# Performance work log

Measured on AMD Instinct MI355X. Metric: run time of the kernel, lower is better.

The kernel has to match this reference:

```python
import jax, jax.numpy as jnp
import numpy as np

B, S, D = 2, 1024, 2048
H, KV, HD = 16, 4, 128
GROUPS = H // KV
THETA = 10000.0


def act_quant(xr, xi):
    # per-token 8-bit absmax quantization over last dim, joint scale for re/im, STE
    amax = jnp.maximum(jnp.max(jnp.abs(xr), -1, keepdims=True),
                       jnp.max(jnp.abs(xi), -1, keepdims=True))
    s = 127.0 / jnp.maximum(amax, 1e-5)
    qr = jnp.clip(jnp.round(xr * s), -128, 127) / s
    qi = jnp.clip(jnp.round(xi * s), -128, 127) / s
    return xr + jax.lax.stop_gradient(qr - xr), xi + jax.lax.stop_gradient(qi - xi)


def weight_quant(wr, wi):
    # Fairy+-i direction quantization: each weight -> scale * d, d in {+1,-1,+i,-i}; STE
    mag = jnp.mean(jnp.sqrt(wr * wr + wi * wi))
    use_re = jnp.abs(wr) >= jnp.abs(wi)
    qr = jnp.where(use_re, jnp.sign(wr) * mag, 0.0)
    qi = jnp.where(use_re, 0.0, jnp.sign(wi) * mag)
    return wr + jax.lax.stop_gradient(qr - wr), wi + jax.lax.stop_gradient(qi - wi)


def complex_linear(xr, xi, wr, wi):
    xr, xi = act_quant(xr, xi)
    wr, wi = weight_quant(wr, wi)
    o_re = xr @ wr - xi @ wi
    o_im = xr @ wi + xi @ wr
    return o_re, o_im


def rotate_half(x):
    h = x.shape[-1] // 2
    return jnp.concatenate([-x[..., h:], x[..., :h]], axis=-1)


def rope_tables():
    inv_freq = 1.0 / (THETA ** (jnp.arange(0, HD, 2, dtype=jnp.float32) / HD))
    pos = jnp.arange(S, dtype=jnp.float32)
    freqs = pos[:, None] * inv_freq[None, :]          # [S, HD/2]
    emb = jnp.concatenate([freqs, freqs], axis=-1)    # [S, HD]
    return jnp.cos(emb)[None, None], jnp.sin(emb)[None, None]  # [1,1,S,HD]


def _heads(x, n):
    # [B,S,n*HD] -> [B,n,S,HD]
    return x.reshape(B, S, n, HD).transpose(0, 2, 1, 3)


def _attn(hidden_real, hidden_imag, wq_re, wq_im, wk_re, wk_im,
          wv_re, wv_im, wo_re, wo_im):
    q_re, q_im = complex_linear(hidden_real, hidden_imag, wq_re, wq_im)
    k_re, k_im = complex_linear(hidden_real, hidden_imag, wk_re, wk_im)
    v_re, v_im = complex_linear(hidden_real, hidden_imag, wv_re, wv_im)

    q_re, q_im = _heads(q_re, H), _heads(q_im, H)      # [B,H,S,HD]
    k_re, k_im = _heads(k_re, KV), _heads(k_im, KV)    # [B,KV,S,HD]
    v_re, v_im = _heads(v_re, KV), _heads(v_im, KV)

    cos, sin = rope_tables()
    # RoPE applied only to real components of q and k
    q_re = q_re * cos + rotate_half(q_re) * sin
    k_re = k_re * cos + rotate_half(k_re) * sin

    # GQA repeat
    k_re = jnp.repeat(k_re, GROUPS, axis=1)
    k_im = jnp.repeat(k_im, GROUPS, axis=1)
    v_re = jnp.repeat(v_re, GROUPS, axis=1)
    v_im = jnp.repeat(v_im, GROUPS, axis=1)

    # real scores = Re(q . conj(k)) = q_re.k_re + q_im.k_im
    scores = (jnp.einsum('bhqd,bhkd->bhqk', q_re, k_re) +
              jnp.einsum('bhqd,bhkd->bhqk', q_im, k_im)) / jnp.sqrt(jnp.float32(HD))
    causal = jnp.tril(jnp.ones((S, S), dtype=bool))
    scores = jnp.where(causal[None, None], scores, jnp.finfo(scores.dtype).min)
    attn = jax.nn.softmax(scores, axis=-1)

    o_re = jnp.einsum('bhqk,bhkd->bhqd', attn, v_re)
    o_im = jnp.einsum('bhqk,bhkd->bhqd', attn, v_im)
    o_re = o_re.transpose(0, 2, 1, 3).reshape(B, S, H * HD)
    o_im = o_im.transpose(0, 2, 1, 3).reshape(B, S, H * HD)

    out_re, out_im = complex_linear(o_re, o_im, wo_re, wo_im)
    return jnp.stack([out_re, out_im])  # [2,B,S,D]


def setup_inputs() -> dict:
    key = jax.random.key(0)
    ks = jax.random.split(key, 12)
    w = lambda k, shp: jax.random.normal(k, shp, dtype=jnp.float32) * 0.02
    return {
        'hidden_real': jax.random.normal(ks[0], (B, S, D), dtype=jnp.float32),
        'hidden_imag': jax.random.normal(ks[1], (B, S, D), dtype=jnp.float32),
        'wq_re': w(ks[2], (D, H * HD)), 'wq_im': w(ks[3], (D, H * HD)),
        'wk_re': w(ks[4], (D, KV * HD)), 'wk_im': w(ks[5], (D, KV * HD)),
        'wv_re': w(ks[6], (D, KV * HD)), 'wv_im': w(ks[7], (D, KV * HD)),
        'wo_re': w(ks[8], (H * HD, D)), 'wo_im': w(ks[9], (H * HD, D)),
    }


def reference(hidden_real, hidden_imag, wq_re, wq_im, wk_re, wk_im,
              wv_re, wv_im, wo_re, wo_im):
    return _attn(hidden_real, hidden_imag, wq_re, wq_im, wk_re, wk_im,
                 wv_re, wv_im, wo_re, wo_im)
```

## Files before the change

### kernel.cpp

```cpp
#include <hip/hip_runtime.h>
#include <stdint.h>

#define B_   2
#define S_   1024
#define D_   2048
#define H_   16
#define KV_  4
#define HD_  128
#define NTOK (B_ * S_)
#define QD   (H_ * HD_)
#define KD   (KV_ * HD_)

using i32x4  = __attribute__((ext_vector_type(4)))  int;
using i32x16 = __attribute__((ext_vector_type(16))) int;
using f32x4  = __attribute__((ext_vector_type(4)))  float;
using bf16x8 = __attribute__((ext_vector_type(8)))  short;

#define LN1E4_OVER_64 0.14391156831212725f

__device__ __forceinline__ float bf2f(uint16_t u) { return __uint_as_float((uint32_t)u << 16); }
__device__ __forceinline__ uint16_t f2bf(float f) {
    uint32_t u = __float_as_uint(f);
    return (uint16_t)((u + 0x7FFFu + ((u >> 16) & 1u)) >> 16);
}

__global__ __launch_bounds__(256)
void act_quant_i8_kernel(const float* __restrict__ xr, const float* __restrict__ xi,
                         int8_t* __restrict__ qr, int8_t* __restrict__ qi,
                         float* __restrict__ invs)
{
    const int tok = blockIdx.x, t = threadIdx.x;
    const float* pr = xr + (size_t)tok * 2048 + t * 8;
    const float* pi = xi + (size_t)tok * 2048 + t * 8;
    float4 r0 = *(const float4*)pr, r1 = *(const float4*)(pr + 4);
    float4 i0 = *(const float4*)pi, i1 = *(const float4*)(pi + 4);
    float am = fmaxf(fmaxf(fmaxf(fabsf(r0.x), fabsf(r0.y)), fmaxf(fabsf(r0.z), fabsf(r0.w))),
                     fmaxf(fmaxf(fabsf(r1.x), fabsf(r1.y)), fmaxf(fabsf(r1.z), fabsf(r1.w))));
    am = fmaxf(am, fmaxf(fmaxf(fmaxf(fabsf(i0.x), fabsf(i0.y)), fmaxf(fabsf(i0.z), fabsf(i0.w))),
                         fmaxf(fmaxf(fabsf(i1.x), fabsf(i1.y)), fmaxf(fabsf(i1.z), fabsf(i1.w)))));
    __shared__ float red[256];
    red[t] = am;
    __syncthreads();
    for (int st = 128; st > 0; st >>= 1) {
        if (t < st) red[t] = fmaxf(red[t], red[t + st]);
        __syncthreads();
    }
    const float s = 127.0f / fmaxf(red[0], 1e-5f);
    if (t == 0) invs[tok] = 1.0f / s;
#define Q8(x) ((uint32_t)(uint8_t)(int8_t)(int)fminf(fmaxf(rintf((x) * s), -128.f), 127.f))
    uint32_t a0 = Q8(r0.x) | (Q8(r0.y) << 8) | (Q8(r0.z) << 16) | (Q8(r0.w) << 24);
    uint32_t a1 = Q8(r1.x) | (Q8(r1.y) << 8) | (Q8(r1.z) << 16) | (Q8(r1.w) << 24);
    uint32_t b0 = Q8(i0.x) | (Q8(i0.y) << 8) | (Q8(i0.z) << 16) | (Q8(i0.w) << 24);
    uint32_t b1 = Q8(i1.x) | (Q8(i1.y) << 8) | (Q8(i1.z) << 16) | (Q8(i1.w) << 24);
#undef Q8
    *(uint32_t*)(qr + (size_t)tok * 2048 + t * 8)     = a0;
    *(uint32_t*)(qr + (size_t)tok * 2048 + t * 8 + 4) = a1;
    *(uint32_t*)(qi + (size_t)tok * 2048 + t * 8)     = b0;
    *(uint32_t*)(qi + (size_t)tok * 2048 + t * 8 + 4) = b1;
}

__global__ __launch_bounds__(256)
void decode_kernel(const float* __restrict__ wr, const float* __restrict__ wi,
                   int N, int8_t* __restrict__ psr, int8_t* __restrict__ psi,
                   int8_t* __restrict__ pnsi, int n_off, float* __restrict__ mag_out)
{
    __shared__ alignas(16) int8_t tr[3][64][80];
    __shared__ float red[256];
    const int n0 = blockIdx.x * 64, k0 = blockIdx.y * 64;
    float msum = 0.f;
    for (int idx = threadIdx.x; idx < 4096; idx += 256) {
        int j = idx & 63, i = idx >> 6;
        size_t g = (size_t)(k0 + i) * N + n0 + j;
        float a = wr[g], b = wi[g];
        msum += sqrtf(a * a + b * b);
        int8_t sr, si;
        if (fabsf(a) >= fabsf(b)) {
            sr = (a > 0.f) ? 1 : ((a < 0.f) ? -1 : 0);
            si = 0;
        } else {
            sr = 0;
            si = (b > 0.f) ? 1 : ((b < 0.f) ? -1 : 0);
        }
        tr[0][j][i] = sr;
        tr[1][j][i] = si;
        tr[2][j][i] = (int8_t)(-si);
    }
    red[threadIdx.x] = msum;
    __syncthreads();
    for (int st = 128; st > 0; st >>= 1) {
        if (threadIdx.x < st) red[threadIdx.x] += red[threadIdx.x + st];
        __syncthreads();
    }
    if (threadIdx.x == 0) atomicAdd(mag_out, red[0]);
    int8_t* planes[3] = { psr, psi, pnsi };
    for (int idx = threadIdx.x; idx < 768; idx += 256) {
        int p = idx >> 8, rem = idx & 255, n = rem >> 2, c = rem & 3;
        int4 v = *(const int4*)&tr[p][n][c * 16];
        *(int4*)(planes[p] + (size_t)(n_off + n0 + n) * 2048 + k0 + c * 16) = v;
    }
}

__device__ __forceinline__ void async_copy16(const void* g, void* l) {
    __builtin_amdgcn_global_load_lds((const __attribute__((address_space(1))) void*)g,
                                     (__attribute__((address_space(3))) void*)l, 16, 0, 0);
}

template <int MODE>
__global__ __launch_bounds__(512, 4)
void gemm_i8_kernel(const int8_t* __restrict__ axr, const int8_t* __restrict__ axi,
                    const int8_t* __restrict__ bsr, const int8_t* __restrict__ bsi,
                    const int8_t* __restrict__ bnsi,
                    int Nout, const float* __restrict__ invs,
                    const float* __restrict__ mag_sums,
                    float magc0, float magc1, float magc2,
                    float* o_re, float* o_im,
                    uint16_t* kbr, uint16_t* kbi, uint16_t* vbr, uint16_t* vbi)
{
    __shared__ alignas(16) int8_t smem[2][5 * 8192];
    const int tid = threadIdx.x;
    const int wav = tid >> 6, lane = tid & 63;
    const int tileM = blockIdx.y * 128, tileN = blockIdx.x * 128;
    const int wm = wav & 1, wn = wav >> 1;
    const int K = 2048;

    const int8_t* gplane[5] = { axr, axi, bsr, bsi, bnsi };
    const int     rbase[5]  = { tileM, tileM, tileN, tileN, tileN };

    i32x16 acc_re[2] = {};
    i32x16 acc_im[2] = {};

    auto issue_tile = [&](int k0, int buf) {
#pragma unroll
        for (int i = 0; i < 5; ++i) {
            int q = wav + 8 * i;
            int pl = q >> 3, seg = q & 7;
            int c = seg >> 1, m0 = (seg & 1) << 6;
            const int8_t* g = gplane[pl] + (size_t)(rbase[pl] + m0 + lane) * K + k0 + c * 16;
            int8_t* l = &smem[buf][pl * 8192 + (c * 128 + m0) * 16];
            async_copy16(g, l);
        }
    };

    issue_tile(0, 0);
    issue_tile(64, 1);

    for (int k = 0; k < 32; ++k) {
        if (k == 31) { asm volatile("s_waitcnt vmcnt(0)" ::: "memory"); }
        else         { asm volatile("s_waitcnt vmcnt(5)" ::: "memory"); }
        asm volatile("s_barrier" ::: "memory");
        const int8_t* sb = smem[k & 1];
#pragma unroll
        for (int s = 0; s < 2; ++s) {
            const int cc = 2 * s + (lane >> 5);
            const int rA = wm * 64 + (lane & 31);
            const int rB = wn * 32 + (lane & 31);
            i32x4 fxr[2], fxi[2], fsr, fsi, fns;
#pragma unroll
            for (int mb = 0; mb < 2; ++mb) {
                int off = (cc * 128 + rA + mb * 32) * 16;
                fxr[mb] = *(const i32x4*)&sb[0 * 8192 + off];
                fxi[mb] = *(const i32x4*)&sb[1 * 8192 + off];
            }
            {
                int off = (cc * 128 + rB) * 16;
                fsr = *(const i32x4*)&sb[2 * 8192 + off];
                fsi = *(const i32x4*)&sb[3 * 8192 + off];
                fns = *(const i32x4*)&sb[4 * 8192 + off];
            }
#pragma unroll
            for (int mb = 0; mb < 2; ++mb) {
                acc_re[mb] = __builtin_amdgcn_mfma_i32_32x32x32_i8(fxr[mb], fsr, acc_re[mb], 0, 0, 0);
                acc_re[mb] = __builtin_amdgcn_mfma_i32_32x32x32_i8(fxi[mb], fns, acc_re[mb], 0, 0, 0);
                acc_im[mb] = __builtin_amdgcn_mfma_i32_32x32x32_i8(fxr[mb], fsi, acc_im[mb], 0, 0, 0);
                acc_im[mb] = __builtin_amdgcn_mfma_i32_32x32x32_i8(fxi[mb], fsr, acc_im[mb], 0, 0, 0);
            }
        }
        asm volatile("s_barrier" ::: "memory");
        if (k + 2 < 32) issue_tile((k + 2) * 64, k & 1);
    }

    const int ln31 = lane & 31, lq = lane >> 5;
    const int gn = tileN + wn * 32 + ln31;
    float mag;
    if (MODE == 0)
        mag = (gn < 2048) ? mag_sums[0] * magc0
            : (gn < 2560) ? mag_sums[1] * magc1
                          : mag_sums[2] * magc2;
    else
        mag = mag_sums[0] * magc0;
#pragma unroll
    for (int mb = 0; mb < 2; ++mb) {
#pragma unroll
        for (int r = 0; r < 16; ++r) {
            const int row = (r & 3) + 8 * (r >> 2) + 4 * lq;
            const int gm = tileM + wm * 64 + mb * 32 + row;
            const float sc = mag * invs[gm];
            const float re = (float)acc_re[mb][r] * sc;
            const float im = (float)acc_im[mb][r] * sc;
            if (MODE == 1) {
                o_re[(size_t)gm * Nout + gn] = re;
                o_im[(size_t)gm * Nout + gn] = im;
            } else {
                const int s = gm & (S_ - 1), bb = gm >> 10;
                if (gn < 2048) {
                    o_re[(size_t)gm * 2048 + gn] = re;
                    o_im[(size_t)gm * 2048 + gn] = im;
                } else if (gn < 2560) {
                    int c = gn - 2048, kvh = c >> 7, d = c & 127;
                    size_t off = ((size_t)(bb * KV_ + kvh) * S_ + s) * 128 + d;
                    kbr[off] = f2bf(re);
                    kbi[off] = f2bf(im);
                } else {
                    int c = gn - 2560, kvh = c >> 7, d = c & 127;
                    size_t off = ((size_t)(bb * KV_ + kvh) * S_ + s) * 128 + d;
                    vbr[off] = f2bf(re);
                    vbi[off] = f2bf(im);
                }
            }
        }
    }
}

__global__ __launch_bounds__(256)
void rope_q_kernel(const float* __restrict__ q_re, const float* __restrict__ q_im,
                   uint16_t* __restrict__ qb_re, uint16_t* __restrict__ qb_im)
{
    int gidx = blockIdx.x * 256 + threadIdx.x;
    int j = gidx & 15, h = (gidx >> 4) & 15, tok = gidx >> 8;
    int s = tok & (S_ - 1), b = tok >> 10;
    int d0 = j * 4;
    size_t ib = (size_t)tok * 2048 + h * 128;
    float4 r0 = *(const float4*)&q_re[ib + d0];
    float4 r1 = *(const float4*)&q_re[ib + d0 + 64];
    float4 i0 = *(const float4*)&q_im[ib + d0];
    float4 i1 = *(const float4*)&q_im[ib + d0 + 64];
    float ro0[4], ro1[4];
    float rv0[4] = { r0.x, r0.y, r0.z, r0.w };
    float rv1[4] = { r1.x, r1.y, r1.z, r1.w };
#pragma unroll
    for (int t = 0; t < 4; ++t) {
        float f = __expf(-(float)(d0 + t) * LN1E4_OVER_64);
        float sn, c;
        __sincosf((float)s * f, &sn, &c);
        ro0[t] = rv0[t] * c - rv1[t] * sn;
        ro1[t] = rv1[t] * c + rv0[t] * sn;
    }
    size_t ob = ((size_t)(b * H_ + h) * S_ + s) * 128;
    ushort4 w;
    w = (ushort4){ f2bf(ro0[0]), f2bf(ro0[1]), f2bf(ro0[2]), f2bf(ro0[3]) };
    *(ushort4*)&qb_re[ob + d0] = w;
    w = (ushort4){ f2bf(ro1[0]), f2bf(ro1[1]), f2bf(ro1[2]), f2bf(ro1[3]) };
    *(ushort4*)&qb_re[ob + d0 + 64] = w;
    w = (ushort4){ f2bf(i0.x), f2bf(i0.y), f2bf(i0.z), f2bf(i0.w) };
    *(ushort4*)&qb_im[ob + d0] = w;
    w = (ushort4){ f2bf(i1.x), f2bf(i1.y), f2bf(i1.z), f2bf(i1.w) };
    *(ushort4*)&qb_im[ob + d0 + 64] = w;
}

__global__ __launch_bounds__(256)
void rope_k_kernel(uint16_t* __restrict__ kb_re)
{
    int gidx = blockIdx.x * 256 + threadIdx.x;
    int j = gidx & 15, kvh = (gidx >> 4) & 3;
    int rest = gidx >> 6;
    int s = rest & (S_ - 1), b = rest >> 10;
    int d0 = j * 4;
    size_t base = ((size_t)(b * KV_ + kvh) * S_ + s) * 128;
    ushort4 u0 = *(const ushort4*)&kb_re[base + d0];
    ushort4 u1 = *(const ushort4*)&kb_re[base + d0 + 64];
    float rv0[4] = { bf2f(u0.x), bf2f(u0.y), bf2f(u0.z), bf2f(u0.w) };
    float rv1[4] = { bf2f(u1.x), bf2f(u1.y), bf2f(u1.z), bf2f(u1.w) };
    float ro0[4], ro1[4];
#pragma unroll
    for (int t = 0; t < 4; ++t) {
        float f = __expf(-(float)(d0 + t) * LN1E4_OVER_64);
        float sn, c;
        __sincosf((float)s * f, &sn, &c);
        ro0[t] = rv0[t] * c - rv1[t] * sn;
        ro1[t] = rv1[t] * c + rv0[t] * sn;
    }
    *(ushort4*)&kb_re[base + d0]      = (ushort4){ f2bf(ro0[0]), f2bf(ro0[1]), f2bf(ro0[2]), f2bf(ro0[3]) };
    *(ushort4*)&kb_re[base + d0 + 64] = (ushort4){ f2bf(ro1[0]), f2bf(ro1[1]), f2bf(ro1[2]), f2bf(ro1[3]) };
}

__global__ __launch_bounds__(256)
void vtrans_kernel(const uint16_t* __restrict__ vbr, const uint16_t* __restrict__ vbi,
                   uint16_t* __restrict__ vtr, uint16_t* __restrict__ vti)
{
    __shared__ uint16_t t[32][36];
    const int pl = blockIdx.z & 1, bk = blockIdx.z >> 1;
    const int s0 = blockIdx.x * 32, d0 = blockIdx.y * 32;
    const uint16_t* src = (pl ? vbi : vbr) + ((size_t)bk * S_) * 128;
    uint16_t*       dst = (pl ? vti : vtr) + ((size_t)bk * 128) * S_;
    const int r = threadIdx.x >> 3, c = (threadIdx.x & 7) * 4;
    *(ushort4*)&t[r][c] = *(const ushort4*)&src[(size_t)(s0 + r) * 128 + d0 + c];
    __syncthreads();
    ushort4 o = (ushort4){ t[c][r], t[c + 1][r], t[c + 2][r], t[c + 3][r] };
    *(ushort4*)&dst[(size_t)(d0 + r) * S_ + s0 + c] = o;
}

__global__ __launch_bounds__(256)
void attn_mfma_kernel(const uint16_t* __restrict__ qb_re, const uint16_t* __restrict__ qb_im,
                      const uint16_t* __restrict__ kb_re, const uint16_t* __restrict__ kb_im,
                      const uint16_t* __restrict__ vt_re, const uint16_t* __restrict__ vt_im,
                      float* __restrict__ o_re, float* __restrict__ o_im)
{
    __shared__ alignas(16) uint16_t sbuf[2][16384];
    __shared__ alignas(16) uint16_t sp[4][16][40];

    const int tid = threadIdx.x;
    const int w = tid >> 6, lane = tid & 63;
    const int r16 = lane & 15, q4 = lane >> 4;
    const int qt = gridDim.x - 1 - blockIdx.x;
    const int h = blockIdx.y, b = blockIdx.z;
    const int kvh = h >> 2;
    const int q0 = qt * 64, qw0 = q0 + w * 16;

    bf16x8 qfr[4], qfi[4];
    {
        const size_t qbase = ((size_t)(b * H_ + h) * S_ + qw0 + r16) * 128;
#pragma unroll
        for (int ks = 0; ks < 4; ++ks) {
            const int col = ks * 32 + q4 * 8;
            qfr[ks] = *(const bf16x8*)&qb_re[qbase + col];
            qfi[ks] = *(const bf16x8*)&qb_im[qbase + col];
        }
    }

    f32x4 oa[2][8] = {};
    float m_r[4] = { -3e38f, -3e38f, -3e38f, -3e38f };
    float l_r[4] = { 0.f, 0.f, 0.f, 0.f };

    const size_t kgbase0 = (size_t)(b * KV_ + kvh) * S_ * 128;
    const uint16_t* vre = vt_re + (size_t)(b * KV_ + kvh) * 128 * (size_t)S_;
    const uint16_t* vim = vt_im + (size_t)(b * KV_ + kvh) * 128 * (size_t)S_;

    const uint16_t* kp[4];
    const uint16_t* vp[4];
#pragma unroll
    for (int i = 0; i < 4; ++i) {
        const int kch = (i & 1) * 8 + w * 2 + (lane >> 5);
        kp[i] = ((i >> 1) ? kb_im : kb_re) + kgbase0 + (size_t)(lane & 31) * 128 + kch * 8;
        const int vch = (i & 1) * 2 + (w >> 1);
        const int vd  = ((w & 1) << 6) | lane;
        vp[i] = ((i >> 1) ? vim : vre) + (size_t)vd * S_ + vch * 8;
    }

    auto issue_tile = [&](int kt, int buf) {
#pragma unroll
        for (int i = 0; i < 4; ++i)
            async_copy16(kp[i] + (size_t)kt * 4096, &sbuf[buf][w * 512 + i * 2048]);
#pragma unroll
        for (int i = 0; i < 4; ++i)
            async_copy16(vp[i] + (size_t)kt * 32, &sbuf[buf][8192 + w * 512 + i * 2048]);
    };

    const int nk = (q0 + 64) >> 5;

    issue_tile(0, 0);
    issue_tile(1, 1);

    for (int k = 0; k < nk; ++k) {
        if (k == nk - 1) { asm volatile("s_waitcnt vmcnt(0)" ::: "memory"); }
        else             { asm volatile("s_waitcnt vmcnt(8)" ::: "memory"); }
        asm volatile("s_barrier" ::: "memory");
        const uint16_t* sb = sbuf[k & 1];
        const int c0 = k << 5;

        if (c0 <= qw0 + 15) {
            f32x4 sc[2] = {};
#pragma unroll
            for (int cblk = 0; cblk < 2; ++cblk) {
                const int krow = cblk * 16 + r16;
#pragma unroll
                for (int ks = 0; ks < 4; ++ks) {
                    const int koff = (ks * 4 + q4) * 256 + krow * 8;
                    bf16x8 kr = *(const bf16x8*)&sb[koff];
                    bf16x8 ki = *(const bf16x8*)&sb[4096 + koff];
                    sc[cblk] = __builtin_amdgcn_mfma_f32_16x16x32_bf16(qfr[ks], kr, sc[cblk], 0, 0, 0);
                    sc[cblk] = __builtin_amdgcn_mfma_f32_16x16x32_bf16(qfi[ks], ki, sc[cblk], 0, 0, 0);
                }
            }
#pragma unroll
            for (int cblk = 0; cblk < 2; ++cblk)
#pragma unroll
                for (int reg = 0; reg < 4; ++reg) {
                    float sval = sc[cblk][reg] * 0.08838834764831845f;
                    const int rowg = qw0 + q4 * 4 + reg;
                    const int colg = c0 + cblk * 16 + r16;
                    if (colg > rowg) sval = -3e38f;
                    sc[cblk][reg] = sval;
                }
            float al[4];
#pragma unroll
            for (int reg = 0; reg < 4; ++reg) {
                float mx = fmaxf(sc[0][reg], sc[1][reg]);
#pragma unroll
                for (int msk = 1; msk < 16; msk <<= 1) mx = fmaxf(mx, __shfl_xor(mx, msk));
                const float mn = fmaxf(m_r[reg], mx);
                al[reg] = __expf(m_r[reg] - mn);
                const float p0 = __expf(sc[0][reg] - mn);
                const float p1 = __expf(sc[1][reg] - mn);
                sc[0][reg] = p0; sc[1][reg] = p1;
                float rs = p0 + p1;
#pragma unroll
                for (int msk = 1; msk < 16; msk <<= 1) rs += __shfl_xor(rs, msk);
                l_r[reg] = l_r[reg] * al[reg] + rs;
                m_r[reg] = mn;
            }
#pragma unroll
            for (int cblk = 0; cblk < 2; ++cblk)
#pragma unroll
                for (int reg = 0; reg < 4; ++reg)
                    sp[w][q4 * 4 + reg][cblk * 16 + r16] = f2bf(sc[cblk][reg]);
#pragma unroll
            for (int dblk = 0; dblk < 8; ++dblk)
#pragma unroll
                for (int reg = 0; reg < 4; ++reg) {
                    oa[0][dblk][reg] *= al[reg];
                    oa[1][dblk][reg] *= al[reg];
                }
            bf16x8 pf = *(const bf16x8*)&sp[w][r16][q4 * 8];
#pragma unroll
            for (int dblk = 0; dblk < 8; ++dblk) {
                const int voff = 8192 + q4 * 1024 + (dblk * 16 + r16) * 8;
                bf16x8 vr = *(const bf16x8*)&sb[voff];
                bf16x8 vi = *(const bf16x8*)&sb[4096 + voff];
                oa[0][dblk] = __builtin_amdgcn_mfma_f32_16x16x32_bf16(pf, vr, oa[0][dblk], 0, 0, 0);
                oa[1][dblk] = __builtin_amdgcn_mfma_f32_16x16x32_bf16(pf, vi, oa[1][dblk], 0, 0, 0);
            }
        }

        asm volatile("s_barrier" ::: "memory");
        if (k + 2 < nk) issue_tile(k + 2, k & 1);
    }

    float inv[4];
#pragma unroll
    for (int reg = 0; reg < 4; ++reg) inv[reg] = 1.f / l_r[reg];
#pragma unroll
    for (int dblk = 0; dblk < 8; ++dblk) {
        const int col = h * 128 + dblk * 16 + r16;
#pragma unroll
        for (int reg = 0; reg < 4; ++reg) {
            const size_t tok = (size_t)b * S_ + qw0 + q4 * 4 + reg;
            o_re[tok * 2048 + col] = oa[0][dblk][reg] * inv[reg];
            o_im[tok * 2048 + col] = oa[1][dblk][reg] * inv[reg];
        }
    }
}

extern "C" void kernel_launch(void* const* d_in, const int* in_sizes, int n_in,
                              void* d_out, int out_size, void* d_ws, size_t ws_size,
                              hipStream_t stream)
{
    const float* hr    = (const float*)d_in[0];
    const float* hi    = (const float*)d_in[1];
    const float* wq_re = (const float*)d_in[2];
    const float* wq_im = (const float*)d_in[3];
    const float* wk_re = (const float*)d_in[4];
    const float* wk_im = (const float*)d_in[5];
    const float* wv_re = (const float*)d_in[6];
    const float* wv_im = (const float*)d_in[7];
    const float* wo_re = (const float*)d_in[8];
    const float* wo_im = (const float*)d_in[9];
    float* out = (float*)d_out;
    char*  base = (char*)d_ws;

    const size_t MB4  = (size_t)2048 * 2048;
    const size_t QKVP = (size_t)3072 * 2048;
    const size_t KVE  = (size_t)B_ * KV_ * S_ * 128;

    float*   mags   = (float*)(base);
    float*   invs1  = (float*)(base + 1024);
    float*   invs2  = (float*)(base + 9216);
    int8_t*  xr_q   = (int8_t*)(base + 32768);
    int8_t*  xi_q   = xr_q + MB4;
    int8_t*  qkv_sr = xi_q + MB4;
    int8_t*  qkv_si = qkv_sr + QKVP;
    int8_t*  qkv_ns = qkv_si + QKVP;
    int8_t*  wo_sr  = qkv_ns + QKVP;
    int8_t*  wo_si  = wo_sr + MB4;
    int8_t*  wo_ns  = wo_si + MB4;
    float*   q_re   = (float*)(wo_ns + MB4);
    float*   q_im   = q_re + MB4;
    uint16_t* kb_re = (uint16_t*)(q_im + MB4);
    uint16_t* kb_im = kb_re + KVE;
    uint16_t* vb_re = kb_im + KVE;
    uint16_t* vb_im = vb_re + KVE;
    uint16_t* vt_re = (uint16_t*)xr_q;
    uint16_t* vt_im = (uint16_t*)xi_q;
    uint16_t* qb_re = (uint16_t*)qkv_sr;
    uint16_t* qb_im = (uint16_t*)(qkv_sr + 8388608);

    hipMemsetAsync(mags, 0, 16, stream);

    decode_kernel<<<dim3(32, 32), 256, 0, stream>>>(wq_re, wq_im, 2048, qkv_sr, qkv_si, qkv_ns, 0,    mags + 0);
    decode_kernel<<<dim3(8, 32),  256, 0, stream>>>(wk_re, wk_im, 512,  qkv_sr, qkv_si, qkv_ns, 2048, mags + 1);
    decode_kernel<<<dim3(8, 32),  256, 0, stream>>>(wv_re, wv_im, 512,  qkv_sr, qkv_si, qkv_ns, 2560, mags + 2);
    decode_kernel<<<dim3(32, 32), 256, 0, stream>>>(wo_re, wo_im, 2048, wo_sr, wo_si, wo_ns, 0,       mags + 3);

    act_quant_i8_kernel<<<NTOK, 256, 0, stream>>>(hr, hi, xr_q, xi_q, invs1);

    gemm_i8_kernel<0><<<dim3(24, 16), 512, 0, stream>>>(
        xr_q, xi_q, qkv_sr, qkv_si, qkv_ns, 0, invs1, mags,
        1.0f / (float)((size_t)D_ * QD), 1.0f / (float)((size_t)D_ * KD), 1.0f / (float)((size_t)D_ * KD),
        q_re, q_im, kb_re, kb_im, vb_re, vb_im);

    rope_q_kernel<<<NTOK * H_ * 16 / 256, 256, 0, stream>>>(q_re, q_im, qb_re, qb_im);
    rope_k_kernel<<<NTOK * KV_ * 16 / 256, 256, 0, stream>>>(kb_re);
    vtrans_kernel<<<dim3(S_ / 32, 128 / 32, B_ * KV_ * 2), 256, 0, stream>>>(vb_re, vb_im, vt_re, vt_im);

    attn_mfma_kernel<<<dim3(S_ / 64, H_, B_), 256, 0, stream>>>(
        qb_re, qb_im, kb_re, kb_im, vt_re, vt_im, q_re, q_im);

    act_quant_i8_kernel<<<NTOK, 256, 0, stream>>>(q_re, q_im, xr_q, xi_q, invs2);

    gemm_i8_kernel<1><<<dim3(16, 16), 512, 0, stream>>>(
        xr_q, xi_q, wo_sr, wo_si, wo_ns, 2048, invs2, mags + 3,
        1.0f / (float)((size_t)QD * D_), 0.f, 0.f,
        out, out + MB4, nullptr, nullptr, nullptr, nullptr);
}
```

Baseline: 486.5 us.

## Drop negated weight plane and retile int8 complex GEMM to 64x128

The decode kernel no longer writes a third negated-imaginary weight plane. The GEMM instead keeps separate accumulators for xr·wr and xi·wi and subtracts them in the epilogue, which cuts weight-plane traffic and LDS footprint per tile. The GEMM tile also shrinks from 128x128 with 512 threads to 64x128 with 256 threads, doubling the grid in M and changing the occupancy hint. The cost is one extra accumulator set per wave, which raises register pressure, and less A/B reuse per block.

```diff
diff --git a/kernel.cpp b/kernel.cpp
--- a/kernel.cpp
+++ b/kernel.cpp
@@ -62,9 +62,9 @@
 __global__ __launch_bounds__(256)
 void decode_kernel(const float* __restrict__ wr, const float* __restrict__ wi,
                    int N, int8_t* __restrict__ psr, int8_t* __restrict__ psi,
-                   int8_t* __restrict__ pnsi, int n_off, float* __restrict__ mag_out)
-{
-    __shared__ alignas(16) int8_t tr[3][64][80];
+                   int n_off, float* __restrict__ mag_out)
+{
+    __shared__ alignas(16) int8_t tr[2][64][80];
     __shared__ float red[256];
     const int n0 = blockIdx.x * 64, k0 = blockIdx.y * 64;
     float msum = 0.f;
@@ -83,7 +83,6 @@
         }
         tr[0][j][i] = sr;
         tr[1][j][i] = si;
-        tr[2][j][i] = (int8_t)(-si);
     }
     red[threadIdx.x] = msum;
     __syncthreads();
@@ -92,8 +91,8 @@
         __syncthreads();
     }
     if (threadIdx.x == 0) atomicAdd(mag_out, red[0]);
-    int8_t* planes[3] = { psr, psi, pnsi };
-    for (int idx = threadIdx.x; idx < 768; idx += 256) {
+    int8_t* planes[2] = { psr, psi };
+    for (int idx = threadIdx.x; idx < 512; idx += 256) {
         int p = idx >> 8, rem = idx & 255, n = rem >> 2, c = rem & 3;
         int4 v = *(const int4*)&tr[p][n][c * 16];
         *(int4*)(planes[p] + (size_t)(n_off + n0 + n) * 2048 + k0 + c * 16) = v;
@@ -106,37 +105,41 @@
 }
 
 template <int MODE>
-__global__ __launch_bounds__(512, 4)
+__global__ __launch_bounds__(256, 3)
 void gemm_i8_kernel(const int8_t* __restrict__ axr, const int8_t* __restrict__ axi,
                     const int8_t* __restrict__ bsr, const int8_t* __restrict__ bsi,
-                    const int8_t* __restrict__ bnsi,
                     int Nout, const float* __restrict__ invs,
                     const float* __restrict__ mag_sums,
                     float magc0, float magc1, float magc2,
                     float* o_re, float* o_im,
                     uint16_t* kbr, uint16_t* kbi, uint16_t* vbr, uint16_t* vbi)
 {
-    __shared__ alignas(16) int8_t smem[2][5 * 8192];
+    __shared__ alignas(16) int8_t smem[2][24576];
     const int tid = threadIdx.x;
     const int wav = tid >> 6, lane = tid & 63;
-    const int tileM = blockIdx.y * 128, tileN = blockIdx.x * 128;
-    const int wm = wav & 1, wn = wav >> 1;
+    const int tileM = blockIdx.y * 64, tileN = blockIdx.x * 128;
     const int K = 2048;
 
-    const int8_t* gplane[5] = { axr, axi, bsr, bsi, bnsi };
-    const int     rbase[5]  = { tileM, tileM, tileN, tileN, tileN };
-
-    i32x16 acc_re[2] = {};
-    i32x16 acc_im[2] = {};
+    i32x16 p1[2] = {};
+    i32x16 p2[2] = {};
+    i32x16 pim[2] = {};
 
     auto issue_tile = [&](int k0, int buf) {
 #pragma unroll
-        for (int i = 0; i < 5; ++i) {
-            int q = wav + 8 * i;
-            int pl = q >> 3, seg = q & 7;
-            int c = seg >> 1, m0 = (seg & 1) << 6;
-            const int8_t* g = gplane[pl] + (size_t)(rbase[pl] + m0 + lane) * K + k0 + c * 16;
-            int8_t* l = &smem[buf][pl * 8192 + (c * 128 + m0) * 16];
+        for (int i = 0; i < 6; ++i) {
+            int q = wav + 4 * i;
+            const int8_t* g;
+            int8_t* l;
+            if (q < 8) {
+                int pl = q >> 2, c = q & 3;
+                g = (pl ? axi : axr) + (size_t)(tileM + lane) * K + k0 + c * 16;
+                l = &smem[buf][pl * 4096 + (c * 64 + lane) * 16];
+            } else {
+                int r = q - 8;
+                int pl = r >> 3, s = r & 7, c = s >> 1, m0 = (s & 1) << 6;
+                g = (pl ? bsi : bsr) + (size_t)(tileN + m0 + lane) * K + k0 + c * 16;
+                l = &smem[buf][8192 + pl * 8192 + (c * 128 + m0 + lane) * 16];
+            }
             async_copy16(g, l);
         }
     };
@@ -146,33 +149,33 @@
 
     for (int k = 0; k < 32; ++k) {
         if (k == 31) { asm volatile("s_waitcnt vmcnt(0)" ::: "memory"); }
-        else         { asm volatile("s_waitcnt vmcnt(5)" ::: "memory"); }
+        else         { asm volatile("s_waitcnt vmcnt(6)" ::: "memory"); }
         asm volatile("s_barrier" ::: "memory");
         const int8_t* sb = smem[k & 1];
 #pragma unroll
         for (int s = 0; s < 2; ++s) {
             const int cc = 2 * s + (lane >> 5);
-            const int rA = wm * 64 + (lane & 31);
-            const int rB = wn * 32 + (lane & 31);
-            i32x4 fxr[2], fxi[2], fsr, fsi, fns;
+            const int rA = lane & 31;
+            const int rB = wav * 32 + (lane & 31);
+            i32x4 fxr[2], fxi[2];
 #pragma unroll
             for (int mb = 0; mb < 2; ++mb) {
-                int off = (cc * 128 + rA + mb * 32) * 16;
-                fxr[mb] = *(const i32x4*)&sb[0 * 8192 + off];
-                fxi[mb] = *(const i32x4*)&sb[1 * 8192 + off];
-            }
+                int off = (cc * 64 + rA + mb * 32) * 16;
+                fxr[mb] = *(const i32x4*)&sb[off];
+                fxi[mb] = *(const i32x4*)&sb[4096 + off];
+            }
+            i32x4 fbr, fbi;
             {
                 int off = (cc * 128 + rB) * 16;
-                fsr = *(const i32x4*)&sb[2 * 8192 + off];
-                fsi = *(const i32x4*)&sb[3 * 8192 + off];
-                fns = *(const i32x4*)&sb[4 * 8192 + off];
+                fbr = *(const i32x4*)&sb[8192 + off];
+                fbi = *(const i32x4*)&sb[16384 + off];
             }
 #pragma unroll
             for (int mb = 0; mb < 2; ++mb) {
-                acc_re[mb] = __builtin_amdgcn_mfma_i32_32x32x32_i8(fxr[mb], fsr, acc_re[mb], 0, 0, 0);
-                acc_re[mb] = __builtin_amdgcn_mfma_i32_32x32x32_i8(fxi[mb], fns, acc_re[mb], 0, 0, 0);
-                acc_im[mb] = __builtin_amdgcn_mfma_i32_32x32x32_i8(fxr[mb], fsi, acc_im[mb], 0, 0, 0);
-                acc_im[mb] = __builtin_amdgcn_mfma_i32_32x32x32_i8(fxi[mb], fsr, acc_im[mb], 0, 0, 0);
+                p1[mb]  = __builtin_amdgcn_mfma_i32_32x32x32_i8(fxr[mb], fbr, p1[mb], 0, 0, 0);
+                p2[mb]  = __builtin_amdgcn_mfma_i32_32x32x32_i8(fxi[mb], fbi, p2[mb], 0, 0, 0);
+                pim[mb] = __builtin_amdgcn_mfma_i32_32x32x32_i8(fxr[mb], fbi, pim[mb], 0, 0, 0);
+                pim[mb] = __builtin_amdgcn_mfma_i32_32x32x32_i8(fxi[mb], fbr, pim[mb], 0, 0, 0);
             }
         }
         asm volatile("s_barrier" ::: "memory");
@@ -180,7 +183,7 @@
     }
 
     const int ln31 = lane & 31, lq = lane >> 5;
-    const int gn = tileN + wn * 32 + ln31;
+    const int gn = tileN + wav * 32 + ln31;
     float mag;
     if (MODE == 0)
         mag = (gn < 2048) ? mag_sums[0] * magc0
@@ -193,10 +196,10 @@
 #pragma unroll
         for (int r = 0; r < 16; ++r) {
             const int row = (r & 3) + 8 * (r >> 2) + 4 * lq;
-            const int gm = tileM + wm * 64 + mb * 32 + row;
+            const int gm = tileM + mb * 32 + row;
             const float sc = mag * invs[gm];
-            const float re = (float)acc_re[mb][r] * sc;
-            const float im = (float)acc_im[mb][r] * sc;
+            const float re = (float)(p1[mb][r] - p2[mb][r]) * sc;
+            const float im = (float)pim[mb][r] * sc;
             if (MODE == 1) {
                 o_re[(size_t)gm * Nout + gn] = re;
                 o_im[(size_t)gm * Nout + gn] = im;
@@ -495,15 +498,15 @@
 
     hipMemsetAsync(mags, 0, 16, stream);
 
-    decode_kernel<<<dim3(32, 32), 256, 0, stream>>>(wq_re, wq_im, 2048, qkv_sr, qkv_si, qkv_ns, 0,    mags + 0);
-    decode_kernel<<<dim3(8, 32),  256, 0, stream>>>(wk_re, wk_im, 512,  qkv_sr, qkv_si, qkv_ns, 2048, mags + 1);
-    decode_kernel<<<dim3(8, 32),  256, 0, stream>>>(wv_re, wv_im, 512,  qkv_sr, qkv_si, qkv_ns, 2560, mags + 2);
-    decode_kernel<<<dim3(32, 32), 256, 0, stream>>>(wo_re, wo_im, 2048, wo_sr, wo_si, wo_ns, 0,       mags + 3);
+    decode_kernel<<<dim3(32, 32), 256, 0, stream>>>(wq_re, wq_im, 2048, qkv_sr, qkv_si, 0,    mags + 0);
+    decode_kernel<<<dim3(8, 32),  256, 0, stream>>>(wk_re, wk_im, 512,  qkv_sr, qkv_si, 2048, mags + 1);
+    decode_kernel<<<dim3(8, 32),  256, 0, stream>>>(wv_re, wv_im, 512,  qkv_sr, qkv_si, 2560, mags + 2);
+    decode_kernel<<<dim3(32, 32), 256, 0, stream>>>(wo_re, wo_im, 2048, wo_sr, wo_si, 0,      mags + 3);
 
     act_quant_i8_kernel<<<NTOK, 256, 0, stream>>>(hr, hi, xr_q, xi_q, invs1);
 
-    gemm_i8_kernel<0><<<dim3(24, 16), 512, 0, stream>>>(
-        xr_q, xi_q, qkv_sr, qkv_si, qkv_ns, 0, invs1, mags,
+    gemm_i8_kernel<0><<<dim3(24, 32), 256, 0, stream>>>(
+        xr_q, xi_q, qkv_sr, qkv_si, 0, invs1, mags,
         1.0f / (float)((size_t)D_ * QD), 1.0f / (float)((size_t)D_ * KD), 1.0f / (float)((size_t)D_ * KD),
         q_re, q_im, kb_re, kb_im, vb_re, vb_im);
 
@@ -516,8 +519,8 @@
 
     act_quant_i8_kernel<<<NTOK, 256, 0, stream>>>(q_re, q_im, xr_q, xi_q, invs2);
 
-    gemm_i8_kernel<1><<<dim3(16, 16), 512, 0, stream>>>(
-        xr_q, xi_q, wo_sr, wo_si, wo_ns, 2048, invs2, mags + 3,
+    gemm_i8_kernel<1><<<dim3(16, 32), 256, 0, stream>>>(
+        xr_q, xi_q, wo_sr, wo_si, 2048, invs2, mags + 3,
         1.0f / (float)((size_t)QD * D_), 0.f, 0.f,
         out, out + MB4, nullptr, nullptr, nullptr, nullptr);
 }
```

After: 469.8 us. 3.4% less time.
